# Kernel optimization log

Hardware: AMD Instinct MI355X
Metric: run time of the kernel (lower is better)

## Reference

```python
import jax, jax.numpy as jnp
import numpy as np

BLOCK_Q = 64
BLOCK_KV = 64
TOPK_RATIO = 0.125


def setup_inputs() -> dict:
    key = jax.random.key(0)
    k1, k2, k3 = jax.random.split(key, 3)
    B, H, L, D = 1, 16, 8192, 64
    q = jax.random.normal(k1, (B, H, L, D), dtype=jnp.float32)
    k = jax.random.normal(k2, (B, H, L, D), dtype=jnp.float32)
    v = jax.random.normal(k3, (B, H, L, D), dtype=jnp.float32)
    return {"q": q, "k": k, "v": v}


def _sparse_lut(q, k):
    # get_sparse_map: block mean-pool q and mean-centered k, score blocks, top-k key blocks
    B, H, L, D = q.shape
    Mb, Nb = L // BLOCK_Q, L // BLOCK_KV
    q_pool = q.reshape(B, H, Mb, BLOCK_Q, D).mean(axis=3)          # [B,H,Mb,D]
    smooth_k = k - k.mean(axis=-2, keepdims=True)
    k_pool = smooth_k.reshape(B, H, Nb, BLOCK_KV, D).mean(axis=3)  # [B,H,Nb,D]
    pred = jnp.einsum('bhmd,bhnd->bhmn', q_pool, k_pool)           # [B,H,Mb,Nb]
    topk = int(TOPK_RATIO * Nb)
    _, lut = jax.lax.top_k(pred, topk)                             # [B,H,Mb,topk]
    return lut


def reference(q, k, v):
    B, H, L, D = q.shape
    Mb, Nb = L // BLOCK_Q, L // BLOCK_KV
    lut = _sparse_lut(q, k)                                        # [B,H,Mb,T] int32
    T = lut.shape[-1]
    sm_scale = D ** -0.5

    kb = k.reshape(B, H, Nb, BLOCK_KV, D)
    vb = v.reshape(B, H, Nb, BLOCK_KV, D)
    bi = jnp.arange(B)[:, None, None, None]
    hi = jnp.arange(H)[None, :, None, None]
    # gather selected KV blocks per query block: [B,H,Mb,T,BLOCK_KV,D]
    k_sel = kb[bi, hi, lut].reshape(B, H, Mb, T * BLOCK_KV, D)
    v_sel = vb[bi, hi, lut].reshape(B, H, Mb, T * BLOCK_KV, D)

    qb = q.reshape(B, H, Mb, BLOCK_Q, D)
    s = jnp.einsum('bhmqd,bhmkd->bhmqk', qb, k_sel) * sm_scale     # [B,H,Mb,BQ,T*BKV]
    p = jax.nn.softmax(s, axis=-1)
    o = jnp.einsum('bhmqk,bhmkd->bhmqd', p, v_sel)
    return o.reshape(B, H, L, D)
```

## Files before the change

kernel.cpp:

```cpp
#include <hip/hip_runtime.h>
#include <hip/hip_bf16.h>


#define H_  16
#define L_  8192
#define D_  64
#define MB_ 128
#define NB_ 128
#define TK_ 16
#define ST_ 72

typedef __bf16 bf16x8 __attribute__((ext_vector_type(8)));
typedef __bf16 bf16x4 __attribute__((ext_vector_type(4)));
typedef short  s16x4  __attribute__((ext_vector_type(4)));
typedef float  f32x4  __attribute__((ext_vector_type(4)));
typedef unsigned short u16x8 __attribute__((ext_vector_type(8)));

union BFU { __hip_bfloat16 h; unsigned short u; };

static __device__ inline unsigned short f2bfu(float f) {
  BFU c; c.h = __float2bfloat16(f); return c.u;
}

static __device__ inline f32x4 mfma16(bf16x4 a, bf16x4 b, f32x4 c) {
#if __has_builtin(__builtin_amdgcn_mfma_f32_16x16x16bf16_1k)
  return __builtin_amdgcn_mfma_f32_16x16x16bf16_1k(
      __builtin_bit_cast(s16x4, a), __builtin_bit_cast(s16x4, b), c, 0, 0, 0);
#elif __has_builtin(__builtin_amdgcn_mfma_f32_16x16x16_bf16)
  return __builtin_amdgcn_mfma_f32_16x16x16_bf16(a, b, c, 0, 0, 0);
#else
  f32x4 d = c;
  asm("v_mfma_f32_16x16x16_bf16 %0, %1, %2, %0" : "+v"(d) : "v"(a), "v"(b));
  return d;
#endif
}

static __device__ inline bf16x4 lo4(bf16x8 v) {
  return __builtin_shufflevector(v, v, 0, 1, 2, 3);
}
static __device__ inline bf16x4 hi4(bf16x8 v) {
  return __builtin_shufflevector(v, v, 4, 5, 6, 7);
}

__device__ unsigned short g_qb[(size_t)H_ * L_ * D_];
__device__ unsigned short g_kf[(size_t)H_ * NB_ * 4096];
__device__ unsigned short g_vf[(size_t)H_ * NB_ * 4096];
__device__ float g_qpool[H_ * NB_ * 64];
__device__ float g_kpool[H_ * NB_ * 64];

static __device__ inline void cvt8_2(const float4& f0, const float4& f1,
                                     unsigned short* dst) {
  u16x8 s;
  s[0] = f2bfu(f0.x); s[1] = f2bfu(f0.y); s[2] = f2bfu(f0.z); s[3] = f2bfu(f0.w);
  s[4] = f2bfu(f1.x); s[5] = f2bfu(f1.y); s[6] = f2bfu(f1.z); s[7] = f2bfu(f1.w);
  *(u16x8*)dst = s;
}

static __device__ inline void cvt8_2s(const float4& f0, const float4& f1,
                                      unsigned short* dst, float sc) {
  u16x8 s;
  s[0] = f2bfu(f0.x * sc); s[1] = f2bfu(f0.y * sc);
  s[2] = f2bfu(f0.z * sc); s[3] = f2bfu(f0.w * sc);
  s[4] = f2bfu(f1.x * sc); s[5] = f2bfu(f1.y * sc);
  s[6] = f2bfu(f1.z * sc); s[7] = f2bfu(f1.w * sc);
  *(u16x8*)dst = s;
}

__global__ __launch_bounds__(256)
void fusedpool_kernel(const float* __restrict__ q,
                      const float* __restrict__ k,
                      const float* __restrict__ v) {
  __shared__ float qt[64 * 64];
  __shared__ float kt[64 * 64];
  __shared__ __align__(16) unsigned short vt_s[64 * ST_];
  __shared__ float pq[4][64], pk[4][64];

  const int b = blockIdx.x;
  const int t = threadIdx.x;
  const int r = t >> 2, c = (t & 3) * 16;
  const size_t base = (size_t)b * 4096 + r * 64 + c;
  const float cs = 0.18033688011112042f;

  float4 qf0 = *(const float4*)(q + base),      qf1 = *(const float4*)(q + base + 4);
  float4 qf2 = *(const float4*)(q + base + 8),  qf3 = *(const float4*)(q + base + 12);
  float4 kf0 = *(const float4*)(k + base),      kf1 = *(const float4*)(k + base + 4);
  float4 kf2 = *(const float4*)(k + base + 8),  kf3 = *(const float4*)(k + base + 12);
  float4 vf0 = *(const float4*)(v + base),      vf1 = *(const float4*)(v + base + 4);
  float4 vf2 = *(const float4*)(v + base + 8),  vf3 = *(const float4*)(v + base + 12);

  cvt8_2s(qf0, qf1, g_qb + base, cs);  cvt8_2s(qf2, qf3, g_qb + base + 8, cs);

  {
    const int w_k = r >> 4, l16k = r & 15;
    const int hf = c >> 5, quadA = (c & 31) >> 3;
    unsigned short* kfp = g_kf + ((size_t)b * 4 + w_k) * 1024 + hf * 512 + l16k * 8;
    cvt8_2(kf0, kf1, kfp + quadA * 128);
    cvt8_2(kf2, kf3, kfp + (quadA + 1) * 128);
  }

  cvt8_2(vf0, vf1, vt_s + r * ST_ + c);
  cvt8_2(vf2, vf3, vt_s + r * ST_ + c + 8);

  *(float4*)(qt + r * 64 + c)      = qf0; *(float4*)(qt + r * 64 + c + 4)  = qf1;
  *(float4*)(qt + r * 64 + c + 8)  = qf2; *(float4*)(qt + r * 64 + c + 12) = qf3;
  *(float4*)(kt + r * 64 + c)      = kf0; *(float4*)(kt + r * 64 + c + 4)  = kf1;
  *(float4*)(kt + r * 64 + c + 8)  = kf2; *(float4*)(kt + r * 64 + c + 12) = kf3;
  __syncthreads();

  const int col = t & 63, g = t >> 6;
  float sq = 0.f, sk = 0.f;
  for (int rr = g * 16; rr < g * 16 + 16; ++rr) {
    sq += qt[rr * 64 + col];
    sk += kt[rr * 64 + col];
  }
  pq[g][col] = sq; pk[g][col] = sk;

  {
    const int wv = t >> 6, lv = t & 63;
    const int l16v = lv & 15, quadv = lv >> 4;
    u16x8 f0, f1;
    #pragma unroll
    for (int n4 = 0; n4 < 2; ++n4)
      #pragma unroll
      for (int rr = 0; rr < 4; ++rr)
        f0[n4 * 4 + rr] = vt_s[(16 * wv + quadv * 4 + rr) * ST_ + 16 * n4 + l16v];
    #pragma unroll
    for (int n4 = 2; n4 < 4; ++n4)
      #pragma unroll
      for (int rr = 0; rr < 4; ++rr)
        f1[(n4 - 2) * 4 + rr] = vt_s[(16 * wv + quadv * 4 + rr) * ST_ + 16 * n4 + l16v];
    unsigned short* vfp = g_vf + ((size_t)b * 4 + wv) * 1024 + lv * 16;
    *(u16x8*)(vfp)     = f0;
    *(u16x8*)(vfp + 8) = f1;
  }

  __syncthreads();
  if (t < 64) {
    g_qpool[b * 64 + t] = (pq[0][t] + pq[1][t] + pq[2][t] + pq[3][t]) * (1.f / 64.f);
    g_kpool[b * 64 + t] = (pk[0][t] + pk[1][t] + pk[2][t] + pk[3][t]) * (1.f / 64.f);
  }
}


__global__ __launch_bounds__(256, 3)
void attn_kernel(float* __restrict__ out) {
  __shared__ float LDSo[4][16][65];
  __shared__ float LDSr[4][64];
  __shared__ int   ls_lut[TK_];

  const int flat = blockIdx.x;
  const int h = (flat & 7) * 2 + ((flat >> 10) & 1);
  const int m = (flat >> 3) & 127;
  const int t = threadIdx.x;
  const int w = t >> 6;
  const int lane = t & 63;
  const int l16 = lane & 15, quad = lane >> 4;

  const unsigned short* qg = g_qb + ((size_t)h * L_ + (size_t)m * 64) * D_;
  bf16x8 qb0[4], qb1[4];
  #pragma unroll
  for (int g = 0; g < 4; ++g) {
    const unsigned short* qp = qg + (16 * g + l16) * 64 + quad * 8;
    qb0[g] = *(const bf16x8*)(qp);
    qb1[g] = *(const bf16x8*)(qp + 32);
  }

  if (w == 0) {
    const int b = h * MB_ + m;
    const float4* qrow = (const float4*)(g_qpool + b * 64);
    const float4* k0 = (const float4*)(g_kpool + (h * NB_ + lane) * 64);
    const float4* k1 = (const float4*)(g_kpool + (h * NB_ + lane + 64) * 64);
    float v0 = 0.f, v1 = 0.f;
    for (int i = 0; i < 16; ++i) {
      float4 qv = qrow[i];
      float4 a = k0[i];
      float4 c = k1[i];
      v0 += qv.x * a.x + qv.y * a.y + qv.z * a.z + qv.w * a.w;
      v1 += qv.x * c.x + qv.y * c.y + qv.z * c.z + qv.w * c.w;
    }
    for (int tt = 0; tt < TK_; ++tt) {
      float bv; int bi;
      if (v0 >= v1) { bv = v0; bi = lane; } else { bv = v1; bi = lane + 64; }
      for (int mask = 1; mask < 64; mask <<= 1) {
        float ov = __shfl_xor(bv, mask, 64);
        int   oi = __shfl_xor(bi, mask, 64);
        if (ov > bv || (ov == bv && oi < bi)) { bv = ov; bi = oi; }
      }
      if (lane == 0) ls_lut[tt] = bi;
      if (bi == lane) v0 = -3.0e38f;
      else if (bi == lane + 64) v1 = -3.0e38f;
    }
  }
  __syncthreads();

  f32x4 o[4][4];
  #pragma unroll
  for (int n4 = 0; n4 < 4; ++n4)
    #pragma unroll
    for (int g = 0; g < 4; ++g) o[n4][g] = (f32x4){0.f, 0.f, 0.f, 0.f};
  float lsum[4] = {0.f, 0.f, 0.f, 0.f};

  const unsigned short* kfh = g_kf + (size_t)h * NB_ * 4096;
  const unsigned short* vfh = g_vf + (size_t)h * NB_ * 4096;

  bf16x8 ka0[2], ka1[2], vv01[2], vv23[2];

  {
    const int kb0 = __builtin_amdgcn_readfirstlane(ls_lut[0]);
    const unsigned short* kbp = kfh + ((size_t)kb0 * 4 + w) * 1024;
    ka0[0] = *(const bf16x8*)(kbp + lane * 8);
    ka1[0] = *(const bf16x8*)(kbp + 512 + lane * 8);
    const unsigned short* vbp = vfh + ((size_t)kb0 * 4 + w) * 1024 + lane * 16;
    vv01[0] = *(const bf16x8*)(vbp);
    vv23[0] = *(const bf16x8*)(vbp + 8);
  }

  #pragma unroll
  for (int j = 0; j < TK_; ++j) {
    const int cb = j & 1, nb = cb ^ 1;
    if (j + 1 < TK_) {
      const int kbn = __builtin_amdgcn_readfirstlane(ls_lut[j + 1]);
      const unsigned short* kbp = kfh + ((size_t)kbn * 4 + w) * 1024;
      ka0[nb] = *(const bf16x8*)(kbp + lane * 8);
      ka1[nb] = *(const bf16x8*)(kbp + 512 + lane * 8);
      const unsigned short* vbp = vfh + ((size_t)kbn * 4 + w) * 1024 + lane * 16;
      vv01[nb] = *(const bf16x8*)(vbp);
      vv23[nb] = *(const bf16x8*)(vbp + 8);
    }

    f32x4 acc[4];
    __builtin_amdgcn_s_setprio(1);
    #pragma unroll
    for (int g = 0; g < 4; ++g) {
      f32x4 z = (f32x4){0.f, 0.f, 0.f, 0.f};
      z = __builtin_amdgcn_mfma_f32_16x16x32_bf16(ka0[cb], qb0[g], z, 0, 0, 0);
      z = __builtin_amdgcn_mfma_f32_16x16x32_bf16(ka1[cb], qb1[g], z, 0, 0, 0);
      acc[g] = z;
    }
    __builtin_amdgcn_s_setprio(0);

    bf16x4 pb[4];
    #pragma unroll
    for (int g = 0; g < 4; ++g) {
      const float p0 = exp2f(acc[g][0]), p1 = exp2f(acc[g][1]);
      const float p2 = exp2f(acc[g][2]), p3 = exp2f(acc[g][3]);
      lsum[g] += (p0 + p1) + (p2 + p3);
      unsigned int d0, d1;
      asm("v_cvt_pk_bf16_f32 %0, %1, %2" : "=v"(d0) : "v"(p0), "v"(p1));
      asm("v_cvt_pk_bf16_f32 %0, %1, %2" : "=v"(d1) : "v"(p2), "v"(p3));
      uint2 dd; dd.x = d0; dd.y = d1;
      pb[g] = __builtin_bit_cast(bf16x4, dd);
    }

    const bf16x4 va_[4] = { lo4(vv01[cb]), hi4(vv01[cb]),
                            lo4(vv23[cb]), hi4(vv23[cb]) };
    __builtin_amdgcn_s_setprio(1);
    #pragma unroll
    for (int n4 = 0; n4 < 4; ++n4)
      #pragma unroll
      for (int g = 0; g < 4; ++g)
        o[n4][g] = mfma16(va_[n4], pb[g], o[n4][g]);
    __builtin_amdgcn_s_setprio(0);
  }

  #pragma unroll
  for (int g = 0; g < 4; ++g) {
    float rs = lsum[g];
    rs += __shfl_xor(rs, 16, 64);
    rs += __shfl_xor(rs, 32, 64);
    lsum[g] = rs;
  }
  if (quad == 0) {
    #pragma unroll
    for (int g = 0; g < 4; ++g) LDSr[w][16 * g + l16] = lsum[g];
  }
  __syncthreads();

  const int dr = t & 15, q0 = (t >> 4) * 4;
  float rinv[4];
  #pragma unroll
  for (int qq = 0; qq < 4; ++qq)
    rinv[qq] = 1.0f / (LDSr[0][q0 + qq] + LDSr[1][q0 + qq] +
                       LDSr[2][q0 + qq] + LDSr[3][q0 + qq]);

  const size_t obase = ((size_t)h * L_ + (size_t)m * 64) * D_;
  #pragma unroll
  for (int n4 = 0; n4 < 4; ++n4) {
    #pragma unroll
    for (int g = 0; g < 4; ++g)
      #pragma unroll
      for (int r = 0; r < 4; ++r)
        LDSo[w][quad * 4 + r][16 * g + l16] = o[n4][g][r];
    __syncthreads();
    #pragma unroll
    for (int qq = 0; qq < 4; ++qq) {
      const int qv = q0 + qq;
      const float s = LDSo[0][dr][qv] + LDSo[1][dr][qv] +
                      LDSo[2][dr][qv] + LDSo[3][dr][qv];
      out[obase + (size_t)qv * 64 + n4 * 16 + dr] = s * rinv[qq];
    }
    __syncthreads();
  }
}

extern "C" void kernel_launch(void* const* d_in, const int* in_sizes, int n_in,
                              void* d_out, int out_size, void* d_ws, size_t ws_size,
                              hipStream_t stream) {
  const float* q = (const float*)d_in[0];
  const float* k = (const float*)d_in[1];
  const float* v = (const float*)d_in[2];
  float* out = (float*)d_out;

  fusedpool_kernel<<<H_ * NB_, 256, 0, stream>>>(q, k, v);
  attn_kernel<<<H_ * MB_, 256, 0, stream>>>(out);
}
```

Baseline: 230.2 us.

## Spread block scoring across threads and interleave top-k selection with KV loop

Block-score dot products are now computed by 128 threads (one key block each) instead of a single wave computing two each, and the scores are shared through LDS. Each wave then runs the top-k argmax rounds itself, one per iteration just before prefetching the next KV block, instead of wave 0 finishing all 16 rounds before the attention loop starts. This removes the serial top-k phase that left three waves idle and overlaps the selection with MFMA work. The cost is that every wave repeats the shuffle reductions, adding redundant cross-lane work inside the main loop.

```diff
diff --git a/kernel.cpp b/kernel.cpp
--- a/kernel.cpp
+++ b/kernel.cpp
@@ -146,7 +146,7 @@
 void attn_kernel(float* __restrict__ out) {
   __shared__ float LDSo[4][16][65];
   __shared__ float LDSr[4][64];
-  __shared__ int   ls_lut[TK_];
+  __shared__ float sc_s[NB_];
 
   const int flat = blockIdx.x;
   const int h = (flat & 7) * 2 + ((flat >> 10) & 1);
@@ -165,33 +165,21 @@
     qb1[g] = *(const bf16x8*)(qp + 32);
   }
 
-  if (w == 0) {
+  if (t < NB_) {
     const int b = h * MB_ + m;
-    const float4* qrow = (const float4*)(g_qpool + b * 64);
-    const float4* k0 = (const float4*)(g_kpool + (h * NB_ + lane) * 64);
-    const float4* k1 = (const float4*)(g_kpool + (h * NB_ + lane + 64) * 64);
-    float v0 = 0.f, v1 = 0.f;
+    const float4* qrow4 = (const float4*)(g_qpool + b * 64);
+    const float4* kp = (const float4*)(g_kpool + (h * NB_ + t) * 64);
+    float s0 = 0.f;
     for (int i = 0; i < 16; ++i) {
-      float4 qv = qrow[i];
-      float4 a = k0[i];
-      float4 c = k1[i];
-      v0 += qv.x * a.x + qv.y * a.y + qv.z * a.z + qv.w * a.w;
-      v1 += qv.x * c.x + qv.y * c.y + qv.z * c.z + qv.w * c.w;
-    }
-    for (int tt = 0; tt < TK_; ++tt) {
-      float bv; int bi;
-      if (v0 >= v1) { bv = v0; bi = lane; } else { bv = v1; bi = lane + 64; }
-      for (int mask = 1; mask < 64; mask <<= 1) {
-        float ov = __shfl_xor(bv, mask, 64);
-        int   oi = __shfl_xor(bi, mask, 64);
-        if (ov > bv || (ov == bv && oi < bi)) { bv = ov; bi = oi; }
-      }
-      if (lane == 0) ls_lut[tt] = bi;
-      if (bi == lane) v0 = -3.0e38f;
-      else if (bi == lane + 64) v1 = -3.0e38f;
-    }
+      float4 qv = qrow4[i];
+      float4 a = kp[i];
+      s0 += qv.x * a.x + qv.y * a.y + qv.z * a.z + qv.w * a.w;
+    }
+    sc_s[t] = s0;
   }
   __syncthreads();
+
+  float sv0 = sc_s[lane], sv1 = sc_s[lane + 64];
 
   f32x4 o[4][4];
   #pragma unroll
@@ -203,10 +191,24 @@
   const unsigned short* kfh = g_kf + (size_t)h * NB_ * 4096;
   const unsigned short* vfh = g_vf + (size_t)h * NB_ * 4096;
 
+  auto argmax_round = [&]() -> int {
+    float bv; int bi;
+    if (sv0 >= sv1) { bv = sv0; bi = lane; } else { bv = sv1; bi = lane + 64; }
+    #pragma unroll
+    for (int mask = 1; mask < 64; mask <<= 1) {
+      float ov = __shfl_xor(bv, mask, 64);
+      int   oi = __shfl_xor(bi, mask, 64);
+      if (ov > bv || (ov == bv && oi < bi)) { bv = ov; bi = oi; }
+    }
+    if (bi == lane) sv0 = -3.0e38f;
+    else if (bi == lane + 64) sv1 = -3.0e38f;
+    return __builtin_amdgcn_readfirstlane(bi);
+  };
+
   bf16x8 ka0[2], ka1[2], vv01[2], vv23[2];
 
   {
-    const int kb0 = __builtin_amdgcn_readfirstlane(ls_lut[0]);
+    const int kb0 = argmax_round();
     const unsigned short* kbp = kfh + ((size_t)kb0 * 4 + w) * 1024;
     ka0[0] = *(const bf16x8*)(kbp + lane * 8);
     ka1[0] = *(const bf16x8*)(kbp + 512 + lane * 8);
@@ -219,7 +221,7 @@
   for (int j = 0; j < TK_; ++j) {
     const int cb = j & 1, nb = cb ^ 1;
     if (j + 1 < TK_) {
-      const int kbn = __builtin_amdgcn_readfirstlane(ls_lut[j + 1]);
+      const int kbn = argmax_round();
       const unsigned short* kbp = kfh + ((size_t)kbn * 4 + w) * 1024;
       ka0[nb] = *(const bf16x8*)(kbp + lane * 8);
       ka1[nb] = *(const bf16x8*)(kbp + 512 + lane * 8);
```

After: 477.2 us. 107% more time.
